# Performance work log

Hardware: AMD Instinct MI355X
Metric: run time of the kernel (lower is better)

## Reference

```python
import jax, jax.numpy as jnp
import numpy as np

D_MODEL = 1024
NUM_HEADS = 16
HEAD_DIM = D_MODEL // NUM_HEADS
B, S = 2, 2048


def setup_inputs() -> dict:
    key = jax.random.key(0)
    ks = jax.random.split(key, 10)
    sc = 1.0 / np.sqrt(D_MODEL)
    return {
        "x": jax.random.normal(ks[0], (B, S, D_MODEL), jnp.float32),
        "y": jax.random.normal(ks[1], (B, S, D_MODEL), jnp.float32),
        "Wkv": jax.random.normal(ks[2], (D_MODEL, 2 * D_MODEL), jnp.float32) * sc,
        "bkv": jax.random.normal(ks[3], (2 * D_MODEL,), jnp.float32) * 0.01,
        "Wq": jax.random.normal(ks[4], (D_MODEL, D_MODEL), jnp.float32) * sc,
        "bq": jax.random.normal(ks[5], (D_MODEL,), jnp.float32) * 0.01,
        "Wo": jax.random.normal(ks[6], (D_MODEL, D_MODEL), jnp.float32) * sc,
        "bo": jax.random.normal(ks[7], (D_MODEL,), jnp.float32) * 0.01,
    }


def reference(x, y, Wkv, bkv, Wq, bq, Wo, bo):
    b, s, d = x.shape
    # projections: kv from x (keys/values come from encoder side), q from y
    kv = x @ Wkv + bkv                      # [B, S, 2*d_model]
    q = y @ Wq + bq                         # [B, S, d_model]
    kv = kv.reshape(b, s, NUM_HEADS, 2 * HEAD_DIM).transpose(0, 2, 1, 3)  # [B,H,S,2*hd]
    q = q.reshape(b, s, NUM_HEADS, HEAD_DIM).transpose(0, 2, 1, 3)        # [B,H,S,hd]
    k, v = jnp.split(kv, 2, axis=-1)        # each [B,H,S,hd]
    scaled = jnp.einsum("bhqd,bhkd->bhqk", q, k) / np.sqrt(HEAD_DIM)      # [B,H,S,S]
    attention = jax.nn.softmax(scaled, axis=-1)
    values = jnp.einsum("bhqk,bhkd->bhqd", attention, v)                  # [B,H,S,hd]
    values = values.transpose(0, 2, 1, 3).reshape(b, s, d)                # [B,S,d_model]
    return values @ Wo + bo
```

## Files before the change

### kernel.cpp

```cpp
#include <hip/hip_runtime.h>
#include <hip/hip_bf16.h>

typedef __attribute__((ext_vector_type(8))) short short8;
typedef __attribute__((ext_vector_type(4))) short short4v;
typedef __attribute__((ext_vector_type(4))) float f32x4;

#define B_  2
#define S_  2048
#define H_  16
#define HD_ 64
#define D_  1024
#define QSCALE 0.18033688f

__device__ __forceinline__ short f2bs(float f) {
  union { float f; unsigned u; } c; c.f = f;
  unsigned u = c.u;
  u += 0x7fffu + ((u >> 16) & 1u);
  return (short)(u >> 16);
}

__device__ __forceinline__ unsigned pack_bf16(float a, float b) {
  __hip_bfloat162 h = __float22bfloat162_rn(float2{a, b});
  return *reinterpret_cast<unsigned*>(&h);
}

__device__ __forceinline__ float fexp2(float x) {
#if __has_builtin(__builtin_amdgcn_exp2f)
  return __builtin_amdgcn_exp2f(x);
#else
  return exp2f(x);
#endif
}

__device__ __forceinline__ float frcp(float x) {
#if __has_builtin(__builtin_amdgcn_rcpf)
  return __builtin_amdgcn_rcpf(x);
#else
  return 1.0f / x;
#endif
}

#define GL2LDS(gp, lp) __builtin_amdgcn_global_load_lds( \
    (const __attribute__((address_space(1))) unsigned int*)(gp), \
    (__attribute__((address_space(3))) unsigned int*)(lp), 16, 0, 0)

__global__ __launch_bounds__(256) void cvt2_kernel(const float* __restrict__ a,
                                                   const float* __restrict__ b,
                                                   short* __restrict__ oa,
                                                   short* __restrict__ ob, int n4each) {
  int i = blockIdx.x * 256 + threadIdx.x;
  const float4* src;
  short4v* dst;
  int j;
  if (i < n4each) { src = (const float4*)a; dst = (short4v*)oa; j = i; }
  else            { src = (const float4*)b; dst = (short4v*)ob; j = i - n4each; }
  float4 f = src[j];
  short4v o;
  o.x = f2bs(f.x); o.y = f2bs(f.y); o.z = f2bs(f.z); o.w = f2bs(f.w);
  dst[j] = o;
}

__global__ __launch_bounds__(256) void trcvt_kernel(const float* __restrict__ in,
                                                    short* __restrict__ out, int R, int C) {
  __shared__ float tile[64][65];
  const int tx = threadIdx.x & 63;
  const int ty = threadIdx.x >> 6;
  const int c0 = blockIdx.x * 64, r0 = blockIdx.y * 64;
#pragma unroll
  for (int i = 0; i < 16; ++i) {
    int r = ty + i * 4;
    tile[r][tx] = in[(size_t)(r0 + r) * C + c0 + tx];
  }
  __syncthreads();
#pragma unroll
  for (int i = 0; i < 16; ++i) {
    int r = ty + i * 4;
    out[(size_t)(c0 + r) * R + r0 + tx] = f2bs(tile[tx][r]);
  }
}

__global__ __launch_bounds__(256) void trcvt2_kernel(const float* __restrict__ in0, short* __restrict__ out0,
                                                     const float* __restrict__ in1, short* __restrict__ out1) {
  __shared__ float tile[64][65];
  const float* in = blockIdx.z ? in1 : in0;
  short* out = blockIdx.z ? out1 : out0;
  const int tx = threadIdx.x & 63;
  const int ty = threadIdx.x >> 6;
  const int c0 = blockIdx.x * 64, r0 = blockIdx.y * 64;
#pragma unroll
  for (int i = 0; i < 16; ++i) {
    int r = ty + i * 4;
    tile[r][tx] = in[(size_t)(r0 + r) * 1024 + c0 + tx];
  }
  __syncthreads();
#pragma unroll
  for (int i = 0; i < 16; ++i) {
    int r = ty + i * 4;
    out[(size_t)(c0 + r) * 1024 + r0 + tx] = f2bs(tile[tx][r]);
  }
}

template <int MODE>
__device__ __forceinline__ void gemm_body(const short* __restrict__ A, const short* __restrict__ Bt,
                                          const float* __restrict__ bias,
                                          void* __restrict__ out0, void* __restrict__ out1,
                                          int m0, int n0, int K, short* smem) {
  short* As = smem;
  short* Bs = smem + 4096;
  const int tid = threadIdx.x;
  const int w = tid >> 6, lane = tid & 63;
  const int q15 = lane & 15, quad = lane >> 4;
  const int wm = (w >> 1) * 64, wn = (w & 1) * 64;

  f32x4 acc[4][4];
#pragma unroll
  for (int i = 0; i < 4; ++i)
#pragma unroll
    for (int j = 0; j < 4; ++j) acc[i][j] = f32x4{0.f, 0.f, 0.f, 0.f};

  const int srow = w * 16 + (lane >> 2);
  const int gch  = (lane & 3) ^ ((lane >> 3) & 3);
  const short* Ag = A + (size_t)(m0 + srow) * K + gch * 8;
  const short* Bg = Bt + (size_t)(n0 + srow) * K + gch * 8;
  short* Al = As + srow * 32 + (lane & 3) * 8;
  short* Bl = Bs + srow * 32 + (lane & 3) * 8;

  for (int kt = 0; kt < K; kt += 32) {
    GL2LDS(Ag + kt,                  Al);
    GL2LDS(Ag + kt + (size_t)64 * K, Al + 64 * 32);
    GL2LDS(Bg + kt,                  Bl);
    GL2LDS(Bg + kt + (size_t)64 * K, Bl + 64 * 32);
    __syncthreads();
    short8 af[4], bf[4];
#pragma unroll
    for (int mi = 0; mi < 4; ++mi) {
      int rr = wm + mi * 16 + q15;
      af[mi] = *(const short8*)(As + rr * 32 + ((quad ^ ((rr >> 1) & 3)) * 8));
    }
#pragma unroll
    for (int ni = 0; ni < 4; ++ni) {
      int rr = wn + ni * 16 + q15;
      bf[ni] = *(const short8*)(Bs + rr * 32 + ((quad ^ ((rr >> 1) & 3)) * 8));
    }
#pragma unroll
    for (int mi = 0; mi < 4; ++mi)
#pragma unroll
      for (int ni = 0; ni < 4; ++ni)
        acc[mi][ni] = __builtin_amdgcn_mfma_f32_16x16x32_bf16(af[mi], bf[ni], acc[mi][ni], 0, 0, 0);
    __syncthreads();
  }

  if constexpr (MODE == 0) {
#pragma unroll
    for (int mi = 0; mi < 4; ++mi)
#pragma unroll
      for (int ni = 0; ni < 4; ++ni) {
        const int n = n0 + wn + ni * 16 + q15;
        const float bn = bias[n];
#pragma unroll
        for (int r = 0; r < 4; ++r) {
          const int m = m0 + wm + mi * 16 + quad * 4 + r;
          int b = m >> 11, s = m & 2047, hh = n >> 6, d = n & 63;
          ((short*)out0)[((size_t)((b * H_ + hh) * S_ + s) << 6) + d] = f2bs((acc[mi][ni][r] + bn) * QSCALE);
        }
      }
  } else {
    const int hh = n0 >> 7;
    const int bb = m0 >> 11;
    const size_t bh = (size_t)(bb * H_ + hh);
    const int s0 = m0 & 2047;
    if ((w & 1) == 0) {
#pragma unroll
      for (int mi = 0; mi < 4; ++mi)
#pragma unroll
        for (int ni = 0; ni < 4; ++ni) {
          const float bn = bias[n0 + ni * 16 + q15];
#pragma unroll
          for (int r = 0; r < 4; ++r) {
            const int s = s0 + wm + mi * 16 + quad * 4 + r;
            ((short*)out0)[((bh * S_ + s) << 6) + ni * 16 + q15] = f2bs(acc[mi][ni][r] + bn);
          }
        }
    } else {
      short* VT = smem;
#pragma unroll
      for (int mi = 0; mi < 4; ++mi)
#pragma unroll
        for (int ni = 0; ni < 4; ++ni) {
          const int d = ni * 16 + q15;
          const float bn = bias[n0 + 64 + ni * 16 + q15];
#pragma unroll
          for (int t = 0; t < 2; ++t) {
            const int chunk = (wm >> 1) + mi * 8 + quad * 2 + t;
            unsigned pk = pack_bf16(acc[mi][ni][2 * t] + bn, acc[mi][ni][2 * t + 1] + bn);
            *reinterpret_cast<unsigned*>(VT + d * 128 + ((chunk ^ (d & 15)) * 2)) = pk;
          }
        }
    }
    __syncthreads();
    {
      short* VT = smem;
      const int d = tid >> 2, t4 = tid & 3;
      unsigned vals[16];
#pragma unroll
      for (int c = 0; c < 16; ++c) {
        int chunk = t4 * 16 + c;
        vals[c] = *reinterpret_cast<unsigned*>(VT + d * 128 + ((chunk ^ (d & 15)) * 2));
      }
      uint4* dst = (uint4*)((short*)out1 + ((bh * HD_ + d) << 11) + s0 + t4 * 32);
      dst[0] = uint4{vals[0], vals[1], vals[2], vals[3]};
      dst[1] = uint4{vals[4], vals[5], vals[6], vals[7]};
      dst[2] = uint4{vals[8], vals[9], vals[10], vals[11]};
      dst[3] = uint4{vals[12], vals[13], vals[14], vals[15]};
    }
  }
}

__global__ __launch_bounds__(256)
void proj_kernel(const short* __restrict__ xb, const short* __restrict__ Wkvt,
                 const float* __restrict__ bkv, short* __restrict__ Kb, short* __restrict__ Vtb,
                 const short* __restrict__ yb, const short* __restrict__ Wqt,
                 const float* __restrict__ bq, short* __restrict__ Qb) {
  __shared__ __align__(16) short smem[8192];
  int bx = blockIdx.x;
  if (bx < 512)
    gemm_body<1>(xb, Wkvt, bkv, Kb, Vtb, (bx >> 4) * 128, (bx & 15) * 128, 1024, smem);
  else {
    bx -= 512;
    gemm_body<0>(yb, Wqt, bq, Qb, nullptr, (bx >> 3) * 128, (bx & 7) * 128, 1024, smem);
  }
}

__global__ __launch_bounds__(256)
void gemm_o_kernel(const short* __restrict__ A, const short* __restrict__ Bt,
                   const float* __restrict__ bias, float* __restrict__ out) {
  __shared__ __align__(16) short As[2048];
  __shared__ __align__(16) short Bs[2048];
  const int tid = threadIdx.x;
  const int w = tid >> 6, lane = tid & 63;
  const int q15 = lane & 15, quad = lane >> 4;
  const int m0 = blockIdx.y * 64, n0 = blockIdx.x * 64;
  const int wm = (w >> 1) * 32, wn = (w & 1) * 32;

  f32x4 acc[2][2];
#pragma unroll
  for (int i = 0; i < 2; ++i)
#pragma unroll
    for (int j = 0; j < 2; ++j) acc[i][j] = f32x4{0.f, 0.f, 0.f, 0.f};

  const int row = tid >> 2;
  const int gch = (tid & 3) ^ ((tid >> 3) & 3);
  const short* Ag = A + (size_t)(m0 + row) * 1024 + gch * 8;
  const short* Bg = Bt + (size_t)(n0 + row) * 1024 + gch * 8;
  short* Al = As + tid * 8;
  short* Bl = Bs + tid * 8;

  for (int kt = 0; kt < 1024; kt += 32) {
    GL2LDS(Ag + kt, Al);
    GL2LDS(Bg + kt, Bl);
    __syncthreads();
    short8 af[2], bf[2];
#pragma unroll
    for (int mi = 0; mi < 2; ++mi) {
      int rr = wm + mi * 16 + q15;
      af[mi] = *(const short8*)(As + rr * 32 + ((quad ^ ((rr >> 1) & 3)) * 8));
    }
#pragma unroll
    for (int ni = 0; ni < 2; ++ni) {
      int rr = wn + ni * 16 + q15;
      bf[ni] = *(const short8*)(Bs + rr * 32 + ((quad ^ ((rr >> 1) & 3)) * 8));
    }
#pragma unroll
    for (int mi = 0; mi < 2; ++mi)
#pragma unroll
      for (int ni = 0; ni < 2; ++ni)
        acc[mi][ni] = __builtin_amdgcn_mfma_f32_16x16x32_bf16(af[mi], bf[ni], acc[mi][ni], 0, 0, 0);
    __syncthreads();
  }

#pragma unroll
  for (int mi = 0; mi < 2; ++mi)
#pragma unroll
    for (int ni = 0; ni < 2; ++ni) {
      const int n = n0 + wn + ni * 16 + q15;
      const float bn = bias[n];
#pragma unroll
      for (int r = 0; r < 4; ++r) {
        const int m = m0 + wm + mi * 16 + quad * 4 + r;
        out[(size_t)m * 1024 + n] = acc[mi][ni][r] + bn;
      }
    }
}

#define PST 72
__global__ __launch_bounds__(256)
void attn_kernel(const short* __restrict__ Q, const short* __restrict__ K,
                 const short* __restrict__ Vt, short* __restrict__ Out) {
  __shared__ __align__(16) short lds[12800];
  short* Ks = lds;
  short* Vs = lds + 4096;
  short* QP = lds + 8192;
  const int tid = threadIdx.x;
  const int w = tid >> 6, lane = tid & 63;
  const int q15 = lane & 15, quad = lane >> 4;
  const int bx = blockIdx.x;
  const int xcd = bx & 7, slot = bx >> 3;
  const int pp = xcd * 4 + (slot >> 5);
  const int qt = slot & 31;
  const int h = pp & 15, b = pp >> 4;
  const size_t bh = (size_t)(b * H_ + h);
  const short* Qg = Q + bh * (S_ * HD_) + qt * (64 * HD_);
  const short* Kg = K + bh * (S_ * HD_);
  const short* Vg = Vt + bh * (HD_ * S_);

  const int srow = w * 8 + (lane >> 3);
  const int gch  = (lane & 7) ^ (srow & 7);

  {
    const short* g = Qg + srow * 64 + gch * 8;
    short* l = QP + w * 512 + lane * 8;
    GL2LDS(g, l);
    GL2LDS(g + 32 * 64, l + 2048);
  }
  __syncthreads();
  short8 aq[2];
  {
    const int rq = w * 16 + q15;
#pragma unroll
    for (int kk = 0; kk < 2; ++kk)
      aq[kk] = *(const short8*)(QP + rq * 64 + (((kk * 4 + quad) ^ (q15 & 7)) * 8));
  }
  short* Psw = QP + w * (16 * PST);

  f32x4 oacc[4];
#pragma unroll
  for (int ni = 0; ni < 4; ++ni) oacc[ni] = f32x4{0.f, 0.f, 0.f, 0.f};
  float lsum = 0.f;

  const short* kg = Kg + srow * 64 + gch * 8;
  short* kl = Ks + w * 512 + lane * 8;
  const short* vg = Vg + (size_t)srow * S_ + gch * 8;
  short* vl = Vs + w * 512 + lane * 8;

  for (int kt = 0; kt < S_ / 64; ++kt) {
    __syncthreads();
    GL2LDS(kg + kt * 4096,        kl);
    GL2LDS(kg + kt * 4096 + 2048, kl + 2048);
    GL2LDS(vg + kt * 64,                   vl);
    GL2LDS(vg + kt * 64 + (size_t)32 * S_, vl + 32 * 64);
    __syncthreads();

    f32x4 sacc[4];
#pragma unroll
    for (int mi = 0; mi < 4; ++mi) sacc[mi] = f32x4{0.f, 0.f, 0.f, 0.f};
#pragma unroll
    for (int mi = 0; mi < 4; ++mi) {
      const int rr = mi * 16 + q15;
#pragma unroll
      for (int kk = 0; kk < 2; ++kk) {
        short8 ak = *(const short8*)(Ks + rr * 64 + (((kk * 4 + quad) ^ (q15 & 7)) * 8));
        sacc[mi] = __builtin_amdgcn_mfma_f32_16x16x32_bf16(ak, aq[kk], sacc[mi], 0, 0, 0);
      }
    }

#pragma unroll
    for (int mi = 0; mi < 4; ++mi) {
      float p0 = fexp2(sacc[mi][0]), p1 = fexp2(sacc[mi][1]);
      float p2 = fexp2(sacc[mi][2]), p3 = fexp2(sacc[mi][3]);
      lsum += (p0 + p1) + (p2 + p3);
      uint2 pk;
      pk.x = pack_bf16(p0, p1);
      pk.y = pack_bf16(p2, p3);
      *reinterpret_cast<uint2*>(Psw + q15 * PST + mi * 16 + quad * 4) = pk;
    }

    short8 ap[2];
#pragma unroll
    for (int kk = 0; kk < 2; ++kk)
      ap[kk] = *(const short8*)(Psw + q15 * PST + kk * 32 + quad * 8);
#pragma unroll
    for (int ni = 0; ni < 4; ++ni) {
      const int rr = ni * 16 + q15;
#pragma unroll
      for (int kk = 0; kk < 2; ++kk) {
        short8 bv = *(const short8*)(Vs + rr * 64 + (((kk * 4 + quad) ^ (q15 & 7)) * 8));
        oacc[ni] = __builtin_amdgcn_mfma_f32_16x16x32_bf16(ap[kk], bv, oacc[ni], 0, 0, 0);
      }
    }
  }

  lsum += __shfl_xor(lsum, 16);
  lsum += __shfl_xor(lsum, 32);
  float inv[4];
#pragma unroll
  for (int r = 0; r < 4; ++r)
    inv[r] = frcp(__shfl(lsum, quad * 4 + r, 64));

#pragma unroll
  for (int ni = 0; ni < 4; ++ni) {
    const int col = h * HD_ + ni * 16 + q15;
#pragma unroll
    for (int r = 0; r < 4; ++r) {
      const int m = b * S_ + qt * 64 + w * 16 + quad * 4 + r;
      Out[(size_t)m * D_ + col] = f2bs(oacc[ni][r] * inv[r]);
    }
  }
}

extern "C" void kernel_launch(void* const* d_in, const int* in_sizes, int n_in,
                              void* d_out, int out_size, void* d_ws, size_t ws_size,
                              hipStream_t stream) {
  const float* x   = (const float*)d_in[0];
  const float* y   = (const float*)d_in[1];
  const float* Wkv = (const float*)d_in[2];
  const float* bkv = (const float*)d_in[3];
  const float* Wq  = (const float*)d_in[4];
  const float* bq  = (const float*)d_in[5];
  const float* Wo  = (const float*)d_in[6];
  const float* bo  = (const float*)d_in[7];
  float* out = (float*)d_out;

  short* xb   = (short*)d_ws;
  short* yb   = xb + (4 << 20);
  short* Wkvt = yb + (4 << 20);
  short* Wqt  = Wkvt + (2 << 20);
  short* Wot  = Wqt + (1 << 20);
  short* Kb   = Wot + (1 << 20);
  short* Vtb  = Kb + (4 << 20);
  short* Qb   = Vtb + (4 << 20);
  short* AOb  = Qb + (4 << 20);

  cvt2_kernel<<<8192, 256, 0, stream>>>(x, y, xb, yb, 1 << 20);
  trcvt_kernel<<<dim3(32, 16), 256, 0, stream>>>(Wkv, Wkvt, 1024, 2048);
  trcvt2_kernel<<<dim3(16, 16, 2), 256, 0, stream>>>(Wq, Wqt, Wo, Wot);

  proj_kernel<<<768, 256, 0, stream>>>(xb, Wkvt, bkv, Kb, Vtb, yb, Wqt, bq, Qb);
  attn_kernel<<<1024, 256, 0, stream>>>(Qb, Kb, Vtb, AOb);
  gemm_o_kernel<<<dim3(16, 64), 256, 0, stream>>>(AOb, Wot, bo, out);
}
```

Measured before the change: 222.5 us.

## Merge prep kernels, double-buffer attention and output GEMM, widen attention query tile

Folds the three conversion and transpose kernels into one prep kernel, removing two launches. The output-projection GEMM now prefetches the next K=64 tile into a double-buffered LDS slot while the current one is computed, and uses a deeper K step per iteration. The attention kernel gets the same K/V double buffering, handles 128 query rows per block (two 16-row subtiles per wave) so each K/V tile is reused twice, and halves the grid to 512 blocks. Larger LDS and register use per block may lower occupancy, and the smaller grid may leave some compute units underfilled.

```diff
diff --git a/kernel.cpp b/kernel.cpp
--- a/kernel.cpp
+++ b/kernel.cpp
@@ -44,53 +44,35 @@
     (const __attribute__((address_space(1))) unsigned int*)(gp), \
     (__attribute__((address_space(3))) unsigned int*)(lp), 16, 0, 0)
 
-__global__ __launch_bounds__(256) void cvt2_kernel(const float* __restrict__ a,
-                                                   const float* __restrict__ b,
-                                                   short* __restrict__ oa,
-                                                   short* __restrict__ ob, int n4each) {
-  int i = blockIdx.x * 256 + threadIdx.x;
-  const float4* src;
-  short4v* dst;
-  int j;
-  if (i < n4each) { src = (const float4*)a; dst = (short4v*)oa; j = i; }
-  else            { src = (const float4*)b; dst = (short4v*)ob; j = i - n4each; }
-  float4 f = src[j];
-  short4v o;
-  o.x = f2bs(f.x); o.y = f2bs(f.y); o.z = f2bs(f.z); o.w = f2bs(f.w);
-  dst[j] = o;
-}
-
-__global__ __launch_bounds__(256) void trcvt_kernel(const float* __restrict__ in,
-                                                    short* __restrict__ out, int R, int C) {
+__global__ __launch_bounds__(256)
+void prep_kernel(const float* __restrict__ x, const float* __restrict__ y,
+                 short* __restrict__ xb, short* __restrict__ yb,
+                 const float* __restrict__ Wkv, short* __restrict__ Wkvt,
+                 const float* __restrict__ Wq, short* __restrict__ Wqt,
+                 const float* __restrict__ Wo, short* __restrict__ Wot) {
   __shared__ float tile[64][65];
-  const int tx = threadIdx.x & 63;
-  const int ty = threadIdx.x >> 6;
-  const int c0 = blockIdx.x * 64, r0 = blockIdx.y * 64;
+  int bx = blockIdx.x;
+  if (bx < 8192) {
+    int i = bx * 256 + threadIdx.x;
+    const float4* src; short4v* dst; int j;
+    if (i < (1 << 20)) { src = (const float4*)x; dst = (short4v*)xb; j = i; }
+    else               { src = (const float4*)y; dst = (short4v*)yb; j = i - (1 << 20); }
+    float4 f = src[j];
+    short4v o;
+    o.x = f2bs(f.x); o.y = f2bs(f.y); o.z = f2bs(f.z); o.w = f2bs(f.w);
+    dst[j] = o;
+    return;
+  }
+  bx -= 8192;
+  const float* in; short* out; int C, c0, r0;
+  if (bx < 512)      { in = Wkv; out = Wkvt; C = 2048; c0 = (bx & 31) * 64; r0 = (bx >> 5) * 64; }
+  else if (bx < 768) { bx -= 512; in = Wq; out = Wqt; C = 1024; c0 = (bx & 15) * 64; r0 = (bx >> 4) * 64; }
+  else               { bx -= 768; in = Wo; out = Wot; C = 1024; c0 = (bx & 15) * 64; r0 = (bx >> 4) * 64; }
+  const int tx = threadIdx.x & 63, ty = threadIdx.x >> 6;
 #pragma unroll
   for (int i = 0; i < 16; ++i) {
     int r = ty + i * 4;
     tile[r][tx] = in[(size_t)(r0 + r) * C + c0 + tx];
-  }
-  __syncthreads();
-#pragma unroll
-  for (int i = 0; i < 16; ++i) {
-    int r = ty + i * 4;
-    out[(size_t)(c0 + r) * R + r0 + tx] = f2bs(tile[tx][r]);
-  }
-}
-
-__global__ __launch_bounds__(256) void trcvt2_kernel(const float* __restrict__ in0, short* __restrict__ out0,
-                                                     const float* __restrict__ in1, short* __restrict__ out1) {
-  __shared__ float tile[64][65];
-  const float* in = blockIdx.z ? in1 : in0;
-  short* out = blockIdx.z ? out1 : out0;
-  const int tx = threadIdx.x & 63;
-  const int ty = threadIdx.x >> 6;
-  const int c0 = blockIdx.x * 64, r0 = blockIdx.y * 64;
-#pragma unroll
-  for (int i = 0; i < 16; ++i) {
-    int r = ty + i * 4;
-    tile[r][tx] = in[(size_t)(r0 + r) * 1024 + c0 + tx];
   }
   __syncthreads();
 #pragma unroll
@@ -234,13 +216,13 @@
 __global__ __launch_bounds__(256)
 void gemm_o_kernel(const short* __restrict__ A, const short* __restrict__ Bt,
                    const float* __restrict__ bias, float* __restrict__ out) {
-  __shared__ __align__(16) short As[2048];
-  __shared__ __align__(16) short Bs[2048];
+  __shared__ __align__(16) short lds[16384];
   const int tid = threadIdx.x;
   const int w = tid >> 6, lane = tid & 63;
   const int q15 = lane & 15, quad = lane >> 4;
   const int m0 = blockIdx.y * 64, n0 = blockIdx.x * 64;
   const int wm = (w >> 1) * 32, wn = (w & 1) * 32;
+  const int xw = q15 & 7;
 
   f32x4 acc[2][2];
 #pragma unroll
@@ -248,34 +230,49 @@
 #pragma unroll
     for (int j = 0; j < 2; ++j) acc[i][j] = f32x4{0.f, 0.f, 0.f, 0.f};
 
-  const int row = tid >> 2;
-  const int gch = (tid & 3) ^ ((tid >> 3) & 3);
-  const short* Ag = A + (size_t)(m0 + row) * 1024 + gch * 8;
-  const short* Bg = Bt + (size_t)(n0 + row) * 1024 + gch * 8;
-  short* Al = As + tid * 8;
-  short* Bl = Bs + tid * 8;
-
-  for (int kt = 0; kt < 1024; kt += 32) {
-    GL2LDS(Ag + kt, Al);
-    GL2LDS(Bg + kt, Bl);
+  const int srow = w * 8 + (lane >> 3);
+  const int gch  = (lane & 7) ^ (srow & 7);
+  const int loff = w * 512 + lane * 8;
+  const short* Ag = A + (size_t)(m0 + srow) * 1024 + gch * 8;
+  const short* Bg = Bt + (size_t)(n0 + srow) * 1024 + gch * 8;
+
+  GL2LDS(Ag,             lds + loff);
+  GL2LDS(Ag + 32 * 1024, lds + loff + 2048);
+  GL2LDS(Bg,             lds + 8192 + loff);
+  GL2LDS(Bg + 32 * 1024, lds + 8192 + loff + 2048);
+
+  for (int kt = 0; kt < 16; ++kt) {
     __syncthreads();
-    short8 af[2], bf[2];
-#pragma unroll
-    for (int mi = 0; mi < 2; ++mi) {
-      int rr = wm + mi * 16 + q15;
-      af[mi] = *(const short8*)(As + rr * 32 + ((quad ^ ((rr >> 1) & 3)) * 8));
-    }
-#pragma unroll
-    for (int ni = 0; ni < 2; ++ni) {
-      int rr = wn + ni * 16 + q15;
-      bf[ni] = *(const short8*)(Bs + rr * 32 + ((quad ^ ((rr >> 1) & 3)) * 8));
-    }
+    const short* Ac = lds + ((kt & 1) ? 4096 : 0);
+    const short* Bc = lds + 8192 + ((kt & 1) ? 4096 : 0);
+    if (kt < 15) {
+      const short* a2 = Ag + (kt + 1) * 64;
+      const short* b2 = Bg + (kt + 1) * 64;
+      short* ad = lds + ((kt & 1) ? 0 : 4096) + loff;
+      short* bd = lds + 8192 + ((kt & 1) ? 0 : 4096) + loff;
+      GL2LDS(a2,             ad);
+      GL2LDS(a2 + 32 * 1024, ad + 2048);
+      GL2LDS(b2,             bd);
+      GL2LDS(b2 + 32 * 1024, bd + 2048);
+    }
+    short8 af[2][2], bf[2][2];
 #pragma unroll
     for (int mi = 0; mi < 2; ++mi)
 #pragma unroll
+      for (int kk = 0; kk < 2; ++kk)
+        af[mi][kk] = *(const short8*)(Ac + (wm + mi * 16 + q15) * 64 + (((kk * 4 + quad) ^ xw) * 8));
+#pragma unroll
+    for (int ni = 0; ni < 2; ++ni)
+#pragma unroll
+      for (int kk = 0; kk < 2; ++kk)
+        bf[ni][kk] = *(const short8*)(Bc + (wn + ni * 16 + q15) * 64 + (((kk * 4 + quad) ^ xw) * 8));
+#pragma unroll
+    for (int mi = 0; mi < 2; ++mi)
+#pragma unroll
       for (int ni = 0; ni < 2; ++ni)
-        acc[mi][ni] = __builtin_amdgcn_mfma_f32_16x16x32_bf16(af[mi], bf[ni], acc[mi][ni], 0, 0, 0);
-    __syncthreads();
+#pragma unroll
+        for (int kk = 0; kk < 2; ++kk)
+          acc[mi][ni] = __builtin_amdgcn_mfma_f32_16x16x32_bf16(af[mi][kk], bf[ni][kk], acc[mi][ni], 0, 0, 0);
   }
 
 #pragma unroll
@@ -293,116 +290,134 @@
 }
 
 #define PST 72
-__global__ __launch_bounds__(256)
+__global__ __launch_bounds__(256, 3)
 void attn_kernel(const short* __restrict__ Q, const short* __restrict__ K,
                  const short* __restrict__ Vt, short* __restrict__ Out) {
-  __shared__ __align__(16) short lds[12800];
-  short* Ks = lds;
-  short* Vs = lds + 4096;
-  short* QP = lds + 8192;
+  __shared__ __align__(16) short lds[25600];
+  short* QP = lds + 16384;
   const int tid = threadIdx.x;
   const int w = tid >> 6, lane = tid & 63;
   const int q15 = lane & 15, quad = lane >> 4;
+  const int xw = q15 & 7;
   const int bx = blockIdx.x;
   const int xcd = bx & 7, slot = bx >> 3;
-  const int pp = xcd * 4 + (slot >> 5);
-  const int qt = slot & 31;
+  const int pp = xcd * 4 + (slot >> 4);
+  const int qt = slot & 15;
   const int h = pp & 15, b = pp >> 4;
   const size_t bh = (size_t)(b * H_ + h);
-  const short* Qg = Q + bh * (S_ * HD_) + qt * (64 * HD_);
+  const short* Qg = Q + bh * (S_ * HD_) + qt * (128 * HD_);
   const short* Kg = K + bh * (S_ * HD_);
   const short* Vg = Vt + bh * (HD_ * S_);
 
   const int srow = w * 8 + (lane >> 3);
   const int gch  = (lane & 7) ^ (srow & 7);
+  const int loff = w * 512 + lane * 8;
 
   {
-    const short* g = Qg + srow * 64 + gch * 8;
-    short* l = QP + w * 512 + lane * 8;
-    GL2LDS(g, l);
-    GL2LDS(g + 32 * 64, l + 2048);
-  }
+    const short* qg = Qg + srow * 64 + gch * 8;
+#pragma unroll
+    for (int t = 0; t < 4; ++t) GL2LDS(qg + t * 2048, QP + loff + t * 2048);
+  }
+  const short* kg = Kg + srow * 64 + gch * 8;
+  const short* vg = Vg + (size_t)srow * S_ + gch * 8;
+  GL2LDS(kg,                   lds + loff);
+  GL2LDS(kg + 2048,            lds + loff + 2048);
+  GL2LDS(vg,                   lds + 8192 + loff);
+  GL2LDS(vg + (size_t)32 * S_, lds + 8192 + loff + 2048);
   __syncthreads();
-  short8 aq[2];
-  {
-    const int rq = w * 16 + q15;
+
+  short8 aq[2][2];
+#pragma unroll
+  for (int st = 0; st < 2; ++st)
 #pragma unroll
     for (int kk = 0; kk < 2; ++kk)
-      aq[kk] = *(const short8*)(QP + rq * 64 + (((kk * 4 + quad) ^ (q15 & 7)) * 8));
-  }
-  short* Psw = QP + w * (16 * PST);
-
-  f32x4 oacc[4];
-#pragma unroll
-  for (int ni = 0; ni < 4; ++ni) oacc[ni] = f32x4{0.f, 0.f, 0.f, 0.f};
-  float lsum = 0.f;
-
-  const short* kg = Kg + srow * 64 + gch * 8;
-  short* kl = Ks + w * 512 + lane * 8;
-  const short* vg = Vg + (size_t)srow * S_ + gch * 8;
-  short* vl = Vs + w * 512 + lane * 8;
-
-  for (int kt = 0; kt < S_ / 64; ++kt) {
+      aq[st][kk] = *(const short8*)(QP + (w * 32 + st * 16 + q15) * 64 + (((kk * 4 + quad) ^ xw) * 8));
+  short* Ps[2] = { QP + w * 2304, QP + w * 2304 + 1152 };
+
+  f32x4 oacc[2][4];
+#pragma unroll
+  for (int st = 0; st < 2; ++st)
+#pragma unroll
+    for (int ni = 0; ni < 4; ++ni) oacc[st][ni] = f32x4{0.f, 0.f, 0.f, 0.f};
+  float lsum[2] = {0.f, 0.f};
+  const f32x4 zz = {0.f, 0.f, 0.f, 0.f};
+
+  for (int kt = 0; kt < 32; ++kt) {
     __syncthreads();
-    GL2LDS(kg + kt * 4096,        kl);
-    GL2LDS(kg + kt * 4096 + 2048, kl + 2048);
-    GL2LDS(vg + kt * 64,                   vl);
-    GL2LDS(vg + kt * 64 + (size_t)32 * S_, vl + 32 * 64);
-    __syncthreads();
-
-    f32x4 sacc[4];
-#pragma unroll
-    for (int mi = 0; mi < 4; ++mi) sacc[mi] = f32x4{0.f, 0.f, 0.f, 0.f};
+    const short* Kc = lds + ((kt & 1) ? 4096 : 0);
+    const short* Vc = lds + 8192 + ((kt & 1) ? 4096 : 0);
+    if (kt < 31) {
+      const short* k2 = kg + (kt + 1) * 4096;
+      const short* v2 = vg + (kt + 1) * 64;
+      short* kd = lds + ((kt & 1) ? 0 : 4096) + loff;
+      short* vd = lds + 8192 + ((kt & 1) ? 0 : 4096) + loff;
+      GL2LDS(k2,                   kd);
+      GL2LDS(k2 + 2048,            kd + 2048);
+      GL2LDS(v2,                   vd);
+      GL2LDS(v2 + (size_t)32 * S_, vd + 2048);
+    }
+
+    f32x4 sacc[2][4];
 #pragma unroll
     for (int mi = 0; mi < 4; ++mi) {
-      const int rr = mi * 16 + q15;
+      const short* kr = Kc + (mi * 16 + q15) * 64;
+      short8 a0 = *(const short8*)(kr + ((quad ^ xw) * 8));
+      short8 a1 = *(const short8*)(kr + (((quad + 4) ^ xw) * 8));
+#pragma unroll
+      for (int st = 0; st < 2; ++st) {
+        f32x4 t = __builtin_amdgcn_mfma_f32_16x16x32_bf16(a0, aq[st][0], zz, 0, 0, 0);
+        sacc[st][mi] = __builtin_amdgcn_mfma_f32_16x16x32_bf16(a1, aq[st][1], t, 0, 0, 0);
+      }
+    }
+
+#pragma unroll
+    for (int st = 0; st < 2; ++st)
+#pragma unroll
+      for (int mi = 0; mi < 4; ++mi) {
+        float p0 = fexp2(sacc[st][mi][0]), p1 = fexp2(sacc[st][mi][1]);
+        float p2 = fexp2(sacc[st][mi][2]), p3 = fexp2(sacc[st][mi][3]);
+        lsum[st] += (p0 + p1) + (p2 + p3);
+        uint2 pk;
+        pk.x = pack_bf16(p0, p1);
+        pk.y = pack_bf16(p2, p3);
+        *reinterpret_cast<uint2*>(Ps[st] + q15 * PST + mi * 16 + quad * 4) = pk;
+      }
+
+    short8 ap[2][2];
+#pragma unroll
+    for (int st = 0; st < 2; ++st)
+#pragma unroll
+      for (int kk = 0; kk < 2; ++kk)
+        ap[st][kk] = *(const short8*)(Ps[st] + q15 * PST + kk * 32 + quad * 8);
+#pragma unroll
+    for (int ni = 0; ni < 4; ++ni) {
+      const short* vr = Vc + (ni * 16 + q15) * 64;
 #pragma unroll
       for (int kk = 0; kk < 2; ++kk) {
-        short8 ak = *(const short8*)(Ks + rr * 64 + (((kk * 4 + quad) ^ (q15 & 7)) * 8));
-        sacc[mi] = __builtin_amdgcn_mfma_f32_16x16x32_bf16(ak, aq[kk], sacc[mi], 0, 0, 0);
-      }
-    }
-
-#pragma unroll
-    for (int mi = 0; mi < 4; ++mi) {
-      float p0 = fexp2(sacc[mi][0]), p1 = fexp2(sacc[mi][1]);
-      float p2 = fexp2(sacc[mi][2]), p3 = fexp2(sacc[mi][3]);
-      lsum += (p0 + p1) + (p2 + p3);
-      uint2 pk;
-      pk.x = pack_bf16(p0, p1);
-      pk.y = pack_bf16(p2, p3);
-      *reinterpret_cast<uint2*>(Psw + q15 * PST + mi * 16 + quad * 4) = pk;
-    }
-
-    short8 ap[2];
-#pragma unroll
-    for (int kk = 0; kk < 2; ++kk)
-      ap[kk] = *(const short8*)(Psw + q15 * PST + kk * 32 + quad * 8);
+        short8 bv = *(const short8*)(vr + (((kk * 4 + quad) ^ xw) * 8));
+#pragma unroll
+        for (int st = 0; st < 2; ++st)
+          oacc[st][ni] = __builtin_amdgcn_mfma_f32_16x16x32_bf16(ap[st][kk], bv, oacc[st][ni], 0, 0, 0);
+      }
+    }
+  }
+
+#pragma unroll
+  for (int st = 0; st < 2; ++st) {
+    float l = lsum[st];
+    l += __shfl_xor(l, 16);
+    l += __shfl_xor(l, 32);
+    float inv[4];
+#pragma unroll
+    for (int r = 0; r < 4; ++r) inv[r] = frcp(__shfl(l, quad * 4 + r, 64));
 #pragma unroll
     for (int ni = 0; ni < 4; ++ni) {
-      const int rr = ni * 16 + q15;
-#pragma unroll
-      for (int kk = 0; kk < 2; ++kk) {
-        short8 bv = *(const short8*)(Vs + rr * 64 + (((kk * 4 + quad) ^ (q15 & 7)) * 8));
-        oacc[ni] = __builtin_amdgcn_mfma_f32_16x16x32_bf16(ap[kk], bv, oacc[ni], 0, 0, 0);
-      }
-    }
-  }
-
-  lsum += __shfl_xor(lsum, 16);
-  lsum += __shfl_xor(lsum, 32);
-  float inv[4];
-#pragma unroll
-  for (int r = 0; r < 4; ++r)
-    inv[r] = frcp(__shfl(lsum, quad * 4 + r, 64));
-
-#pragma unroll
-  for (int ni = 0; ni < 4; ++ni) {
-    const int col = h * HD_ + ni * 16 + q15;
-#pragma unroll
-    for (int r = 0; r < 4; ++r) {
-      const int m = b * S_ + qt * 64 + w * 16 + quad * 4 + r;
-      Out[(size_t)m * D_ + col] = f2bs(oacc[ni][r] * inv[r]);
+      const int col = h * HD_ + ni * 16 + q15;
+#pragma unroll
+      for (int r = 0; r < 4; ++r) {
+        const int m = b * S_ + qt * 128 + w * 32 + st * 16 + quad * 4 + r;
+        Out[(size_t)m * D_ + col] = f2bs(oacc[st][ni][r] * inv[r]);
+      }
     }
   }
 }
@@ -430,11 +445,8 @@
   short* Qb   = Vtb + (4 << 20);
   short* AOb  = Qb + (4 << 20);
 
-  cvt2_kernel<<<8192, 256, 0, stream>>>(x, y, xb, yb, 1 << 20);
-  trcvt_kernel<<<dim3(32, 16), 256, 0, stream>>>(Wkv, Wkvt, 1024, 2048);
-  trcvt2_kernel<<<dim3(16, 16, 2), 256, 0, stream>>>(Wq, Wqt, Wo, Wot);
-
+  prep_kernel<<<9216, 256, 0, stream>>>(x, y, xb, yb, Wkv, Wkvt, Wq, Wqt, Wo, Wot);
   proj_kernel<<<768, 256, 0, stream>>>(xb, Wkvt, bkv, Kb, Vtb, yb, Wqt, bq, Qb);
-  attn_kernel<<<1024, 256, 0, stream>>>(Qb, Kb, Vtb, AOb);
+  attn_kernel<<<512, 256, 0, stream>>>(Qb, Kb, Vtb, AOb);
   gemm_o_kernel<<<dim3(16, 64), 256, 0, stream>>>(AOb, Wot, bo, out);
 }
```

New measurement: 211.9 us. 1.05x faster.
